# Kernel optimization log

Measured on AMD Instinct MI355X. Metric: run time of the kernel, lower is better.

Reference implementation:

```python
import jax, jax.numpy as jnp
import numpy as np

B, V, E, H, L = 8, 200, 40000, 128, 3


def setup_inputs() -> dict:
    key = jax.random.key(0)
    ks = jax.random.split(key, 24)
    s = 1.0 / np.sqrt(H)
    inp = {
        "x": jax.random.normal(ks[0], (B, V, 2), jnp.float32),
        "e": jax.random.uniform(ks[1], (B, E), jnp.float32),
        "edge_index": jax.random.randint(ks[2], (B, 2, E), 0, V),
        # Embedder
        "node_W": jax.random.normal(ks[3], (2, H), jnp.float32) * 0.5,
        "node_b": jnp.zeros((H,), jnp.float32),
        "edge_W": jax.random.normal(ks[4], (1, H), jnp.float32) * 0.5,
        "edge_b": jnp.zeros((H,), jnp.float32),
        # GCN layers (stacked over L)
        "U_W": jax.random.normal(ks[5], (L, H, H), jnp.float32) * s,
        "U_b": jnp.zeros((L, H), jnp.float32),
        "V_W": jax.random.normal(ks[6], (L, H, H), jnp.float32) * s,
        "V_b": jnp.zeros((L, H), jnp.float32),
        "A_W": jax.random.normal(ks[7], (L, H, H), jnp.float32) * s,
        "A_b": jnp.zeros((L, H), jnp.float32),
        "B_W": jax.random.normal(ks[8], (L, H, H), jnp.float32) * s,
        "B_b": jnp.zeros((L, H), jnp.float32),
        "C_W": jax.random.normal(ks[9], (L, H, H), jnp.float32) * s,
        "C_b": jnp.zeros((L, H), jnp.float32),
        # Out MLP: hidden -> hidden -> 2
        "out_W1": jax.random.normal(ks[10], (H, H), jnp.float32) * s,
        "out_b1": jnp.zeros((H,), jnp.float32),
        "out_W2": jax.random.normal(ks[11], (H, 2), jnp.float32) * s,
        "out_b2": jnp.zeros((2,), jnp.float32),
    }
    return inp


def reference(x, e, edge_index, node_W, node_b, edge_W, edge_b,
              U_W, U_b, V_W, V_b, A_W, A_b, B_W, B_b, C_W, C_b,
              out_W1, out_b1, out_W2, out_b2):
    n_nodes = x.shape[1]
    n_layers = U_W.shape[0]

    def per_graph(xi, ei, idx):
        # Embedder: coords (V,2)->(V,H), distances (E,)->(E,H)
        xh = xi @ node_W + node_b
        eh = ei[:, None] @ edge_W + edge_b
        src, dst = idx[0], idx[1]
        for l in range(n_layers):
            gate = jax.nn.sigmoid(eh)                       # (E,H) edge gates
            vx = xh @ V_W[l] + V_b[l]                       # (V,H)
            agg = jax.ops.segment_sum(gate * vx[src], dst,
                                      num_segments=n_nodes)  # (V,H)
            x_new = xh + jax.nn.relu(xh @ U_W[l] + U_b[l] + agg)
            eh = eh + jax.nn.relu(eh @ A_W[l] + A_b[l]
                                  + (xh @ B_W[l] + B_b[l])[src]
                                  + (xh @ C_W[l] + C_b[l])[dst])
            xh = x_new
        h = jax.nn.relu(eh @ out_W1 + out_b1)
        return jax.nn.sigmoid(h @ out_W2 + out_b2)           # (E,2)

    # batch loop in the original torch code -> vmap here
    return jax.vmap(per_graph)(x, e, edge_index)
```

## Files before the change

### kernel.cpp

```cpp
#include <hip/hip_runtime.h>
#include <hip/hip_bf16.h>

#define NB 8
#define NV 200
#define NE 40000
#define NH 128
#define NL 3
#define EBLK 157

typedef __attribute__((ext_vector_type(8))) __bf16 bf16x8;
typedef __attribute__((ext_vector_type(8))) short s16x8;
typedef __attribute__((ext_vector_type(4))) short s16x4;
typedef __attribute__((ext_vector_type(4))) float f32x4;

__device__ inline float sigmoidf_(float x){ return 1.0f/(1.0f + __expf(-x)); }

__device__ inline short f2b(float f){
  union{ float f; unsigned u; } v; v.f = f;
  unsigned u = v.u;
  u += 0x7fffu + ((u >> 16) & 1u);
  return (short)(u >> 16);
}
__device__ inline float b2f(short s){
  union{ unsigned u; float f; } v; v.u = ((unsigned)(unsigned short)s) << 16;
  return v.f;
}
__device__ inline void splitb(float x, short &hi, short &lo){
  hi = f2b(x);
  lo = f2b(x - b2f(hi));
}

__global__ __launch_bounds__(256) void k_embed_nodes(
    const float* __restrict__ x, const float* __restrict__ nW,
    const float* __restrict__ nb, float* __restrict__ xh)
{
  int i = blockIdx.x*256 + threadIdx.x;
  if (i >= NB*NV*NH) return;
  int h  = i & (NH-1);
  int bv = i >> 7;
  xh[i] = x[bv*2+0]*nW[h] + x[bv*2+1]*nW[NH+h] + nb[h];
}

__global__ __launch_bounds__(256) void k_trans_w(
    const float* __restrict__ AW, const float* __restrict__ oW1,
    short* __restrict__ Wt)
{
  int m = blockIdx.x;
  const float* src = (m < 3) ? (AW + m*NH*NH) : oW1;
  short* dhi = Wt + (size_t)m*NH*NH;
  short* dlo = Wt + (size_t)(4+m)*NH*NH;
  for (int i = threadIdx.x; i < NH*NH; i += 256){
    int n = i >> 7, k = i & 127;
    short hi, lo;
    splitb(src[k*NH + n], hi, lo);
    dhi[i] = hi; dlo[i] = lo;
  }
}

__global__ __launch_bounds__(256) void k_zero(int* __restrict__ p, int n){
  int i = blockIdx.x*256 + threadIdx.x;
  if (i < n) p[i] = 0;
}

__global__ __launch_bounds__(256) void k_count(const int* __restrict__ ei, int* __restrict__ counts){
  int i = blockIdx.x*256 + threadIdx.x;
  if (i >= NB*NE) return;
  int b = i / NE, e = i % NE;
  int dv = ei[b*2*NE + NE + e];
  atomicAdd(&counts[b*NV + dv], 1);
}

__global__ void k_scan(const int* __restrict__ counts, int* __restrict__ offs, int* __restrict__ cursor){
  int b = blockIdx.x;
  if (threadIdx.x == 0){
    int run = 0;
    for (int v=0; v<NV; v++){
      offs[b*(NV+1)+v] = run;
      cursor[b*NV+v]   = run;
      run += counts[b*NV+v];
    }
    offs[b*(NV+1)+NV] = run;
  }
}

__global__ __launch_bounds__(256) void k_scatter(const int* __restrict__ ei, int* __restrict__ cursor, int* __restrict__ csr){
  int i = blockIdx.x*256 + threadIdx.x;
  if (i >= NB*NE) return;
  int b = i / NE, e = i % NE;
  int dv = ei[b*2*NE + NE + e];
  int pos = atomicAdd(&cursor[b*NV + dv], 1);
  csr[(size_t)b*NE + pos] = e;
}

__global__ __launch_bounds__(256) void k_node_mm(
    float* __restrict__ xh, const float* __restrict__ agg,
    const float* __restrict__ VWl, const float* __restrict__ Vbl,
    const float* __restrict__ BWl, const float* __restrict__ Bbl,
    const float* __restrict__ CWl, const float* __restrict__ Cbl,
    const float* __restrict__ UWl, const float* __restrict__ Ubl,
    float* __restrict__ vx, float* __restrict__ bx,
    float* __restrict__ cx, float* __restrict__ ux,
    int do_update)
{
  __shared__ float sx[NH];
  int b = blockIdx.x / NV, v = blockIdx.x % NV;
  size_t row = (size_t)b*NV + v;
  float* xr = xh + row*NH;
  int ht = threadIdx.x;
  if (ht < NH){
    float xv = xr[ht];
    if (do_update){
      float u = ux[row*NH + ht];
      #pragma unroll
      for (int p=0;p<4;p++) u += agg[(size_t)p*NB*NV*NH + row*NH + ht];
      xv += u > 0.f ? u : 0.f;
      xr[ht] = xv;
    }
    sx[ht] = xv;
  }
  __syncthreads();
  #pragma unroll
  for (int pass=0; pass<2; pass++){
    int t = threadIdx.x + pass*256;
    int mat = t >> 7, h = t & 127;
    const float* W = (mat==0) ? VWl : (mat==1) ? BWl : (mat==2) ? CWl : UWl;
    const float* bs = (mat==0) ? Vbl : (mat==1) ? Bbl : (mat==2) ? Cbl : Ubl;
    float* op = (mat==0) ? vx : (mat==1) ? bx : (mat==2) ? cx : ux;
    float acc = bs[h];
    #pragma unroll 8
    for (int k=0;k<NH;k++) acc += sx[k]*W[k*NH + h];
    op[row*NH + h] = acc;
  }
}

__global__ __launch_bounds__(128) void k_agg(
    const float* __restrict__ eh, const float* __restrict__ evec,
    const float* __restrict__ eWe, const float* __restrict__ ebe,
    const float* __restrict__ vx, const int* __restrict__ ei,
    const int* __restrict__ csr, const int* __restrict__ offs,
    float* __restrict__ agg, int is_l0)
{
  int part = blockIdx.x & 3;
  int bv   = blockIdx.x >> 2;
  int b = bv / NV, v = bv % NV;
  int h = threadIdx.x;
  const int* srcp  = ei + b*2*NE;
  const int* csrg  = csr + (size_t)b*NE;
  const float* ehg = eh + (size_t)b*NE*NH;
  const float* evg = evec + (size_t)b*NE;
  const float* vxg = vx + (size_t)b*NV*NH;
  float wh = eWe[h], bh = ebe[h];
  int beg = offs[b*(NV+1)+v], end = offs[b*(NV+1)+v+1];
  int len = end - beg;
  int i    = beg + ((len*part) >> 2);
  int stop = beg + ((len*(part+1)) >> 2);
  float acc = 0.f;
  for (; i+8 <= stop; i += 8){
    int   eb[8], sb[8];
    float a[8], w[8];
    #pragma unroll
    for (int j=0;j<8;j++) eb[j] = csrg[i+j];
    #pragma unroll
    for (int j=0;j<8;j++) sb[j] = srcp[eb[j]];
    if (is_l0){
      #pragma unroll
      for (int j=0;j<8;j++) a[j] = evg[eb[j]]*wh + bh;
    } else {
      #pragma unroll
      for (int j=0;j<8;j++) a[j] = ehg[(size_t)eb[j]*NH + h];
    }
    #pragma unroll
    for (int j=0;j<8;j++) w[j] = vxg[sb[j]*NH + h];
    #pragma unroll
    for (int j=0;j<8;j++) acc += sigmoidf_(a[j]) * w[j];
  }
  for (; i < stop; i++){
    int e0 = csrg[i]; int s0 = srcp[e0];
    float a = is_l0 ? (evg[e0]*wh + bh) : ehg[(size_t)e0*NH+h];
    acc += sigmoidf_(a) * vxg[s0*NH+h];
  }
  agg[((size_t)part*NB*NV + (size_t)b*NV + v)*NH + h] = acc;
}

__global__ __launch_bounds__(512) void k_edge_update(
    float* __restrict__ eh, const short* __restrict__ Wt,
    const float* __restrict__ Ab, const float* __restrict__ bx,
    const float* __restrict__ cx, const int* __restrict__ ei,
    const float* __restrict__ evec, const float* __restrict__ eWe,
    const float* __restrict__ ebe, int is_l0)
{
  __shared__ short sW[2*NH*NH];
  const short* Whi = Wt;
  const short* Wlo = Wt + 4*NH*NH;
  {
    #pragma unroll
    for (int i=0;i<8;i++){
      int sidx = (threadIdx.x + i*512)*8;
      int p = sidx >> 14, r = sidx & 16383;
      int hh = r >> 7, kw = r & 127;
      const short* src = p ? Wlo : Whi;
      s16x8 vv = *(const s16x8*)(src + r);
      *(s16x8*)(sW + p*16384 + hh*128 + (kw ^ ((hh&7)<<3))) = vv;
    }
  }
  __syncthreads();

  int blk  = blockIdx.x % EBLK;
  int b    = blockIdx.x / EBLK;
  int wave = threadIdx.x >> 6;
  int lane = threadIdx.x & 63;
  int l15 = lane & 15, lg = lane >> 4;
  int eA = blk*256 + wave*32 + l15;
  int eB = eA + 16;
  int eAc = eA < NE ? eA : NE-1;
  int eBc = eB < NE ? eB : NE-1;
  float* ehg = eh + (size_t)b*NE*NH;
  const int* srcp = ei + b*2*NE;
  int svA = srcp[eAc], dvA = srcp[NE+eAc];
  int svB = srcp[eBc], dvB = srcp[NE+eBc];

  float evA = 0.f, evB = 0.f;
  f32x4 rA[8], rB[8];
  if (is_l0){
    evA = evec[(size_t)b*NE + eAc];
    evB = evec[(size_t)b*NE + eBc];
    #pragma unroll
    for (int kk=0;kk<4;kk++){
      f32x4 w0 = *(const f32x4*)(eWe + kk*32 + lg*8);
      f32x4 w1 = *(const f32x4*)(eWe + kk*32 + lg*8 + 4);
      f32x4 q0 = *(const f32x4*)(ebe + kk*32 + lg*8);
      f32x4 q1 = *(const f32x4*)(ebe + kk*32 + lg*8 + 4);
      #pragma unroll
      for (int j=0;j<4;j++){
        rA[2*kk][j]   = evA*w0[j] + q0[j];
        rA[2*kk+1][j] = evA*w1[j] + q1[j];
        rB[2*kk][j]   = evB*w0[j] + q0[j];
        rB[2*kk+1][j] = evB*w1[j] + q1[j];
      }
    }
  } else {
    const float* pA = ehg + (size_t)eAc*NH + lg*8;
    const float* pB = ehg + (size_t)eBc*NH + lg*8;
    #pragma unroll
    for (int kk=0;kk<4;kk++){
      rA[2*kk]   = *(const f32x4*)(pA + kk*32);
      rA[2*kk+1] = *(const f32x4*)(pA + kk*32 + 4);
    }
    #pragma unroll
    for (int kk=0;kk<4;kk++){
      rB[2*kk]   = *(const f32x4*)(pB + kk*32);
      rB[2*kk+1] = *(const f32x4*)(pB + kk*32 + 4);
    }
  }

  bf16x8 ahA[4], alA[4], ahB[4], alB[4];
  #pragma unroll
  for (int kk=0;kk<4;kk++){
    union{ short s[8]; bf16x8 v; } uh, ul;
    #pragma unroll
    for (int j=0;j<4;j++){
      splitb(rA[2*kk][j],   uh.s[j],   ul.s[j]);
      splitb(rA[2*kk+1][j], uh.s[4+j], ul.s[4+j]);
    }
    ahA[kk] = uh.v; alA[kk] = ul.v;
  }
  #pragma unroll
  for (int kk=0;kk<4;kk++){
    union{ short s[8]; bf16x8 v; } uh, ul;
    #pragma unroll
    for (int j=0;j<4;j++){
      splitb(rB[2*kk][j],   uh.s[j],   ul.s[j]);
      splitb(rB[2*kk+1][j], uh.s[4+j], ul.s[4+j]);
    }
    ahB[kk] = uh.v; alB[kk] = ul.v;
  }

  f32x4 accA[8], accB[8];
  #pragma unroll
  for (int n=0;n<8;n++){ accA[n] = (f32x4){0.f,0.f,0.f,0.f}; accB[n] = (f32x4){0.f,0.f,0.f,0.f}; }

  #pragma unroll
  for (int kk=0;kk<4;kk++){
    #pragma unroll
    for (int n=0;n<8;n++){
      int row = n*16 + l15;
      int cofs = (kk*32 + lg*8) ^ ((l15&7)<<3);
      union{ s16x8 s; bf16x8 v; } wh, wl;
      wh.s = *(const s16x8*)(sW + row*128 + cofs);
      wl.s = *(const s16x8*)(sW + 16384 + row*128 + cofs);
      accA[n] = __builtin_amdgcn_mfma_f32_16x16x32_bf16(wh.v, ahA[kk], accA[n], 0, 0, 0);
      accA[n] = __builtin_amdgcn_mfma_f32_16x16x32_bf16(wh.v, alA[kk], accA[n], 0, 0, 0);
      accA[n] = __builtin_amdgcn_mfma_f32_16x16x32_bf16(wl.v, ahA[kk], accA[n], 0, 0, 0);
      accB[n] = __builtin_amdgcn_mfma_f32_16x16x32_bf16(wh.v, ahB[kk], accB[n], 0, 0, 0);
      accB[n] = __builtin_amdgcn_mfma_f32_16x16x32_bf16(wh.v, alB[kk], accB[n], 0, 0, 0);
      accB[n] = __builtin_amdgcn_mfma_f32_16x16x32_bf16(wl.v, ahB[kk], accB[n], 0, 0, 0);
    }
  }

  const float* bxA = bx + ((size_t)b*NV + svA)*NH;
  const float* cxA = cx + ((size_t)b*NV + dvA)*NH;
  const float* bxB = bx + ((size_t)b*NV + svB)*NH;
  const float* cxB = cx + ((size_t)b*NV + dvB)*NH;
  float* ehA = ehg + (size_t)eAc*NH;
  float* ehB = ehg + (size_t)eBc*NH;
  #pragma unroll
  for (int n=0;n<8;n++){
    int h0 = n*16 + lg*4;
    f32x4 ab4 = *(const f32x4*)(Ab + h0);
    f32x4 bA = *(const f32x4*)(bxA + h0);
    f32x4 cA = *(const f32x4*)(cxA + h0);
    f32x4 bB = *(const f32x4*)(bxB + h0);
    f32x4 cB = *(const f32x4*)(cxB + h0);
    f32x4 oA, oB;
    if (is_l0){
      f32x4 w4 = *(const f32x4*)(eWe + h0);
      f32x4 q4 = *(const f32x4*)(ebe + h0);
      #pragma unroll
      for (int j=0;j<4;j++){ oA[j] = evA*w4[j] + q4[j]; oB[j] = evB*w4[j] + q4[j]; }
    } else {
      oA = *(const f32x4*)(ehA + h0);
      oB = *(const f32x4*)(ehB + h0);
    }
    f32x4 nA, nB;
    #pragma unroll
    for (int j=0;j<4;j++){
      float vA = accA[n][j] + ab4[j] + bA[j] + cA[j];
      vA = vA > 0.f ? vA : 0.f;
      nA[j] = oA[j] + vA;
      float vB = accB[n][j] + ab4[j] + bB[j] + cB[j];
      vB = vB > 0.f ? vB : 0.f;
      nB[j] = oB[j] + vB;
    }
    if (eA < NE) *(f32x4*)(ehA + h0) = nA;
    if (eB < NE) *(f32x4*)(ehB + h0) = nB;
  }
}

__global__ __launch_bounds__(512) void k_edge_out(
    const float* __restrict__ eh, const short* __restrict__ Wt,
    const float* __restrict__ Ab, const float* __restrict__ bx,
    const float* __restrict__ cx, const int* __restrict__ ei,
    const float* __restrict__ b1, const float* __restrict__ W2,
    const float* __restrict__ b2, float* __restrict__ out)
{
  __shared__ short sW[2*NH*NH];
  const short* Whi = Wt + 2*NH*NH;
  const short* Wlo = Wt + 6*NH*NH;
  {
    #pragma unroll
    for (int i=0;i<8;i++){
      int sidx = (threadIdx.x + i*512)*8;
      int p = sidx >> 14, r = sidx & 16383;
      int hh = r >> 7, kw = r & 127;
      const short* src = p ? Wlo : Whi;
      s16x8 vv = *(const s16x8*)(src + r);
      *(s16x8*)(sW + p*16384 + hh*128 + (kw ^ ((hh&7)<<3))) = vv;
    }
  }
  __syncthreads();

  int blk  = blockIdx.x % EBLK;
  int b    = blockIdx.x / EBLK;
  int wave = threadIdx.x >> 6;
  int lane = threadIdx.x & 63;
  int l15 = lane & 15, lg = lane >> 4;
  int eA = blk*256 + wave*32 + l15;
  int eB = eA + 16;
  int eAc = eA < NE ? eA : NE-1;
  int eBc = eB < NE ? eB : NE-1;
  const float* ehg = eh + (size_t)b*NE*NH;
  const int* srcp = ei + b*2*NE;
  int svA = srcp[eAc], dvA = srcp[NE+eAc];
  int svB = srcp[eBc], dvB = srcp[NE+eBc];

  const float* pA = ehg + (size_t)eAc*NH + lg*8;
  const float* pB = ehg + (size_t)eBc*NH + lg*8;
  f32x4 rA[8], rB[8];
  #pragma unroll
  for (int kk=0;kk<4;kk++){
    rA[2*kk]   = *(const f32x4*)(pA + kk*32);
    rA[2*kk+1] = *(const f32x4*)(pA + kk*32 + 4);
  }
  #pragma unroll
  for (int kk=0;kk<4;kk++){
    rB[2*kk]   = *(const f32x4*)(pB + kk*32);
    rB[2*kk+1] = *(const f32x4*)(pB + kk*32 + 4);
  }

  bf16x8 ahA[4], alA[4], ahB[4], alB[4];
  #pragma unroll
  for (int kk=0;kk<4;kk++){
    union{ short s[8]; bf16x8 v; } uh, ul;
    #pragma unroll
    for (int j=0;j<4;j++){
      splitb(rA[2*kk][j],   uh.s[j],   ul.s[j]);
      splitb(rA[2*kk+1][j], uh.s[4+j], ul.s[4+j]);
    }
    ahA[kk] = uh.v; alA[kk] = ul.v;
  }
  #pragma unroll
  for (int kk=0;kk<4;kk++){
    union{ short s[8]; bf16x8 v; } uh, ul;
    #pragma unroll
    for (int j=0;j<4;j++){
      splitb(rB[2*kk][j],   uh.s[j],   ul.s[j]);
      splitb(rB[2*kk+1][j], uh.s[4+j], ul.s[4+j]);
    }
    ahB[kk] = uh.v; alB[kk] = ul.v;
  }

  f32x4 accA[8], accB[8];
  #pragma unroll
  for (int n=0;n<8;n++){ accA[n] = (f32x4){0.f,0.f,0.f,0.f}; accB[n] = (f32x4){0.f,0.f,0.f,0.f}; }
  #pragma unroll
  for (int kk=0;kk<4;kk++){
    #pragma unroll
    for (int n=0;n<8;n++){
      int row = n*16 + l15;
      int cofs = (kk*32 + lg*8) ^ ((l15&7)<<3);
      union{ s16x8 s; bf16x8 v; } wh, wl;
      wh.s = *(const s16x8*)(sW + row*128 + cofs);
      wl.s = *(const s16x8*)(sW + 16384 + row*128 + cofs);
      accA[n] = __builtin_amdgcn_mfma_f32_16x16x32_bf16(wh.v, ahA[kk], accA[n], 0, 0, 0);
      accA[n] = __builtin_amdgcn_mfma_f32_16x16x32_bf16(wh.v, alA[kk], accA[n], 0, 0, 0);
      accA[n] = __builtin_amdgcn_mfma_f32_16x16x32_bf16(wl.v, ahA[kk], accA[n], 0, 0, 0);
      accB[n] = __builtin_amdgcn_mfma_f32_16x16x32_bf16(wh.v, ahB[kk], accB[n], 0, 0, 0);
      accB[n] = __builtin_amdgcn_mfma_f32_16x16x32_bf16(wh.v, alB[kk], accB[n], 0, 0, 0);
      accB[n] = __builtin_amdgcn_mfma_f32_16x16x32_bf16(wl.v, ahB[kk], accB[n], 0, 0, 0);
    }
  }

  f32x4 nAr[8], nBr[8];
  const float* bxA = bx + ((size_t)b*NV + svA)*NH;
  const float* cxA = cx + ((size_t)b*NV + dvA)*NH;
  const float* bxB = bx + ((size_t)b*NV + svB)*NH;
  const float* cxB = cx + ((size_t)b*NV + dvB)*NH;
  const float* ehA = ehg + (size_t)eAc*NH;
  const float* ehB = ehg + (size_t)eBc*NH;
  #pragma unroll
  for (int n=0;n<8;n++){
    int h0 = n*16 + lg*4;
    f32x4 ab4 = *(const f32x4*)(Ab + h0);
    f32x4 bA = *(const f32x4*)(bxA + h0);
    f32x4 cA = *(const f32x4*)(cxA + h0);
    f32x4 oA = *(const f32x4*)(ehA + h0);
    f32x4 bB = *(const f32x4*)(bxB + h0);
    f32x4 cB = *(const f32x4*)(cxB + h0);
    f32x4 oB = *(const f32x4*)(ehB + h0);
    #pragma unroll
    for (int j=0;j<4;j++){
      float vA = accA[n][j] + ab4[j] + bA[j] + cA[j];
      vA = vA > 0.f ? vA : 0.f;
      nAr[n][j] = oA[j] + vA;
      float vB = accB[n][j] + ab4[j] + bB[j] + cB[j];
      vB = vB > 0.f ? vB : 0.f;
      nBr[n][j] = oB[j] + vB;
    }
  }

  __syncthreads();
  {
    const short* W1hi = Wt + 3*NH*NH;
    const short* W1lo = Wt + 7*NH*NH;
    #pragma unroll
    for (int i=0;i<16;i++){
      int qd = threadIdx.x + i*512;
      int p = qd >> 12, rr = qd & 4095;
      int row = rr >> 5;
      int c0 = (rr & 31) << 2;
      int kk = c0 >> 5, lgs = (c0 >> 3) & 3, jhi = (c0 & 7) >> 2;
      int base = 32*kk + 16*jhi + 4*lgs;
      const short* src = p ? W1lo : W1hi;
      s16x4 v = *(const s16x4*)(src + row*128 + base);
      *(s16x4*)(sW + p*16384 + row*128 + (c0 ^ ((row&7)<<3))) = v;
    }
  }
  __syncthreads();

  bf16x8 qhA[4], qlA[4], qhB[4], qlB[4];
  #pragma unroll
  for (int kk=0;kk<4;kk++){
    union{ short s[8]; bf16x8 v; } uhA, ulA, uhB, ulB;
    #pragma unroll
    for (int j=0;j<8;j++){
      splitb(nAr[2*kk + (j>>2)][j&3], uhA.s[j], ulA.s[j]);
      splitb(nBr[2*kk + (j>>2)][j&3], uhB.s[j], ulB.s[j]);
    }
    qhA[kk] = uhA.v; qlA[kk] = ulA.v;
    qhB[kk] = uhB.v; qlB[kk] = ulB.v;
  }

  f32x4 acc2A[8], acc2B[8];
  #pragma unroll
  for (int n=0;n<8;n++){ acc2A[n] = (f32x4){0.f,0.f,0.f,0.f}; acc2B[n] = (f32x4){0.f,0.f,0.f,0.f}; }
  #pragma unroll
  for (int kk=0;kk<4;kk++){
    #pragma unroll
    for (int n=0;n<8;n++){
      int row = n*16 + l15;
      int cofs = (kk*32 + lg*8) ^ ((l15&7)<<3);
      union{ s16x8 s; bf16x8 v; } wh, wl;
      wh.s = *(const s16x8*)(sW + row*128 + cofs);
      wl.s = *(const s16x8*)(sW + 16384 + row*128 + cofs);
      acc2A[n] = __builtin_amdgcn_mfma_f32_16x16x32_bf16(wh.v, qhA[kk], acc2A[n], 0, 0, 0);
      acc2A[n] = __builtin_amdgcn_mfma_f32_16x16x32_bf16(wh.v, qlA[kk], acc2A[n], 0, 0, 0);
      acc2A[n] = __builtin_amdgcn_mfma_f32_16x16x32_bf16(wl.v, qhA[kk], acc2A[n], 0, 0, 0);
      acc2B[n] = __builtin_amdgcn_mfma_f32_16x16x32_bf16(wh.v, qhB[kk], acc2B[n], 0, 0, 0);
      acc2B[n] = __builtin_amdgcn_mfma_f32_16x16x32_bf16(wh.v, qlB[kk], acc2B[n], 0, 0, 0);
      acc2B[n] = __builtin_amdgcn_mfma_f32_16x16x32_bf16(wl.v, qhB[kk], acc2B[n], 0, 0, 0);
    }
  }

  float p0A = 0.f, p1A = 0.f, p0B = 0.f, p1B = 0.f;
  #pragma unroll
  for (int n=0;n<8;n++){
    int h0 = n*16 + lg*4;
    f32x4 b14 = *(const f32x4*)(b1 + h0);
    f32x4 wA  = *(const f32x4*)(W2 + h0*2);
    f32x4 wB  = *(const f32x4*)(W2 + h0*2 + 4);
    #pragma unroll
    for (int j=0;j<4;j++){
      float w20 = (j<2) ? wA[2*j]   : wB[2*(j-2)];
      float w21 = (j<2) ? wA[2*j+1] : wB[2*(j-2)+1];
      float hA = acc2A[n][j] + b14[j]; hA = hA > 0.f ? hA : 0.f;
      float hB = acc2B[n][j] + b14[j]; hB = hB > 0.f ? hB : 0.f;
      p0A += hA*w20; p1A += hA*w21;
      p0B += hB*w20; p1B += hB*w21;
    }
  }
  p0A += __shfl_xor(p0A, 16, 64); p0A += __shfl_xor(p0A, 32, 64);
  p1A += __shfl_xor(p1A, 16, 64); p1A += __shfl_xor(p1A, 32, 64);
  p0B += __shfl_xor(p0B, 16, 64); p0B += __shfl_xor(p0B, 32, 64);
  p1B += __shfl_xor(p1B, 16, 64); p1B += __shfl_xor(p1B, 32, 64);
  if (lg == 0){
    float bb0 = b2[0], bb1 = b2[1];
    if (eA < NE){
      float2 r; r.x = sigmoidf_(p0A + bb0); r.y = sigmoidf_(p1A + bb1);
      *(float2*)(out + ((size_t)b*NE + eA)*2) = r;
    }
    if (eB < NE){
      float2 r; r.x = sigmoidf_(p0B + bb0); r.y = sigmoidf_(p1B + bb1);
      *(float2*)(out + ((size_t)b*NE + eB)*2) = r;
    }
  }
}

extern "C" void kernel_launch(void* const* d_in, const int* in_sizes, int n_in,
                              void* d_out, int out_size, void* d_ws, size_t ws_size,
                              hipStream_t stream)
{
  const float* x   = (const float*)d_in[0];
  const float* e   = (const float*)d_in[1];
  const int*   ei  = (const int*)d_in[2];
  const float* nW  = (const float*)d_in[3];
  const float* nb  = (const float*)d_in[4];
  const float* eW  = (const float*)d_in[5];
  const float* eb  = (const float*)d_in[6];
  const float* UW  = (const float*)d_in[7];
  const float* Ub  = (const float*)d_in[8];
  const float* VW  = (const float*)d_in[9];
  const float* Vb  = (const float*)d_in[10];
  const float* AW  = (const float*)d_in[11];
  const float* Ab  = (const float*)d_in[12];
  const float* BW  = (const float*)d_in[13];
  const float* Bb  = (const float*)d_in[14];
  const float* CW  = (const float*)d_in[15];
  const float* Cb  = (const float*)d_in[16];
  const float* oW1 = (const float*)d_in[17];
  const float* ob1 = (const float*)d_in[18];
  const float* oW2 = (const float*)d_in[19];
  const float* ob2 = (const float*)d_in[20];
  float* out = (float*)d_out;

  char* ws = (char*)d_ws;
  size_t off = 0;
  auto alloc = [&](size_t bytes)->char*{
    char* p = ws + off;
    off += (bytes + 255) & ~(size_t)255;
    return p;
  };
  float* eh     = (float*)alloc((size_t)NB*NE*NH*4);
  float* xh     = (float*)alloc((size_t)NB*NV*NH*4);
  float* vx     = (float*)alloc((size_t)NB*NV*NH*4);
  float* bx     = (float*)alloc((size_t)NB*NV*NH*4);
  float* cx     = (float*)alloc((size_t)NB*NV*NH*4);
  float* ux     = (float*)alloc((size_t)NB*NV*NH*4);
  float* agg    = (float*)alloc((size_t)4*NB*NV*NH*4);
  short* Wt     = (short*)alloc((size_t)8*NH*NH*2);
  int* counts   = (int*)alloc((size_t)NB*NV*4);
  int* cursor   = (int*)alloc((size_t)NB*NV*4);
  int* offs     = (int*)alloc((size_t)NB*(NV+1)*4);
  int* csr      = (int*)alloc((size_t)NB*NE*4);
  (void)ws_size; (void)in_sizes; (void)n_in; (void)out_size;

  k_embed_nodes<<<(NB*NV*NH+255)/256, 256, 0, stream>>>(x, nW, nb, xh);
  k_trans_w<<<4, 256, 0, stream>>>(AW, oW1, Wt);
  k_zero<<<(NB*NV+255)/256, 256, 0, stream>>>(counts, NB*NV);
  k_count<<<(NB*NE+255)/256, 256, 0, stream>>>(ei, counts);
  k_scan<<<NB, 64, 0, stream>>>(counts, offs, cursor);
  k_scatter<<<(NB*NE+255)/256, 256, 0, stream>>>(ei, cursor, csr);

  for (int l=0; l<NL; l++){
    k_node_mm<<<NB*NV, 256, 0, stream>>>(xh, agg,
        VW + l*NH*NH, Vb + l*NH, BW + l*NH*NH, Bb + l*NH,
        CW + l*NH*NH, Cb + l*NH, UW + l*NH*NH, Ub + l*NH,
        vx, bx, cx, ux, l > 0 ? 1 : 0);
    if (l < NL-1)
      k_agg<<<NB*NV*4, 128, 0, stream>>>(eh, e, eW, eb, vx, ei, csr, offs, agg, l==0 ? 1 : 0);
    if (l < NL-1)
      k_edge_update<<<NB*EBLK, 512, 0, stream>>>(eh, Wt + l*NH*NH, Ab + l*NH, bx, cx, ei,
                                                 e, eW, eb, l==0 ? 1 : 0);
    else
      k_edge_out<<<NB*EBLK, 512, 0, stream>>>(eh, Wt, Ab + l*NH, bx, cx, ei,
                                              ob1, oW2, ob2, out);
  }
}
```

Baseline: 554.7 us.

## Halve edge-block size, keep only hi weights in LDS, read lo weights from global

```diff
diff --git a/kernel.cpp b/kernel.cpp
--- a/kernel.cpp
+++ b/kernel.cpp
@@ -6,11 +6,10 @@
 #define NE 40000
 #define NH 128
 #define NL 3
-#define EBLK 157
+#define EBLK 313
 
 typedef __attribute__((ext_vector_type(8))) __bf16 bf16x8;
 typedef __attribute__((ext_vector_type(8))) short s16x8;
-typedef __attribute__((ext_vector_type(4))) short s16x4;
 typedef __attribute__((ext_vector_type(4))) float f32x4;
 
 __device__ inline float sigmoidf_(float x){ return 1.0f/(1.0f + __expf(-x)); }
@@ -50,7 +49,14 @@
   short* dhi = Wt + (size_t)m*NH*NH;
   short* dlo = Wt + (size_t)(4+m)*NH*NH;
   for (int i = threadIdx.x; i < NH*NH; i += 256){
-    int n = i >> 7, k = i & 127;
+    int n = i >> 7, c = i & 127;
+    int k;
+    if (m < 3){
+      k = c;
+    } else {
+      int kk = c >> 5, lg = (c >> 3) & 3, jh = (c >> 2) & 1, jl = c & 3;
+      k = 32*kk + 16*jh + 4*lg + jl;
+    }
     short hi, lo;
     splitb(src[k*NH + n], hi, lo);
     dhi[i] = hi; dlo[i] = lo;
@@ -182,25 +188,23 @@
   agg[((size_t)part*NB*NV + (size_t)b*NV + v)*NH + h] = acc;
 }
 
-__global__ __launch_bounds__(512) void k_edge_update(
+__global__ __launch_bounds__(256) void k_edge_update(
     float* __restrict__ eh, const short* __restrict__ Wt,
     const float* __restrict__ Ab, const float* __restrict__ bx,
     const float* __restrict__ cx, const int* __restrict__ ei,
     const float* __restrict__ evec, const float* __restrict__ eWe,
     const float* __restrict__ ebe, int is_l0)
 {
-  __shared__ short sW[2*NH*NH];
+  __shared__ short sW[NH*NH];
   const short* Whi = Wt;
   const short* Wlo = Wt + 4*NH*NH;
   {
     #pragma unroll
     for (int i=0;i<8;i++){
-      int sidx = (threadIdx.x + i*512)*8;
-      int p = sidx >> 14, r = sidx & 16383;
-      int hh = r >> 7, kw = r & 127;
-      const short* src = p ? Wlo : Whi;
-      s16x8 vv = *(const s16x8*)(src + r);
-      *(s16x8*)(sW + p*16384 + hh*128 + (kw ^ ((hh&7)<<3))) = vv;
+      int sidx = (threadIdx.x + i*256)*8;
+      int hh = sidx >> 7, kw = sidx & 127;
+      s16x8 vv = *(const s16x8*)(Whi + sidx);
+      *(s16x8*)(sW + hh*128 + (kw ^ ((hh&7)<<3))) = vv;
     }
   }
   __syncthreads();
@@ -210,7 +214,7 @@
   int wave = threadIdx.x >> 6;
   int lane = threadIdx.x & 63;
   int l15 = lane & 15, lg = lane >> 4;
-  int eA = blk*256 + wave*32 + l15;
+  int eA = blk*128 + wave*32 + l15;
   int eB = eA + 16;
   int eAc = eA < NE ? eA : NE-1;
   int eBc = eB < NE ? eB : NE-1;
@@ -287,7 +291,7 @@
       int cofs = (kk*32 + lg*8) ^ ((l15&7)<<3);
       union{ s16x8 s; bf16x8 v; } wh, wl;
       wh.s = *(const s16x8*)(sW + row*128 + cofs);
-      wl.s = *(const s16x8*)(sW + 16384 + row*128 + cofs);
+      wl.s = *(const s16x8*)(Wlo + row*NH + kk*32 + lg*8);
       accA[n] = __builtin_amdgcn_mfma_f32_16x16x32_bf16(wh.v, ahA[kk], accA[n], 0, 0, 0);
       accA[n] = __builtin_amdgcn_mfma_f32_16x16x32_bf16(wh.v, alA[kk], accA[n], 0, 0, 0);
       accA[n] = __builtin_amdgcn_mfma_f32_16x16x32_bf16(wl.v, ahA[kk], accA[n], 0, 0, 0);
@@ -336,25 +340,25 @@
   }
 }
 
-__global__ __launch_bounds__(512) void k_edge_out(
+__global__ __launch_bounds__(256) void k_edge_out(
     const float* __restrict__ eh, const short* __restrict__ Wt,
     const float* __restrict__ Ab, const float* __restrict__ bx,
     const float* __restrict__ cx, const int* __restrict__ ei,
     const float* __restrict__ b1, const float* __restrict__ W2,
     const float* __restrict__ b2, float* __restrict__ out)
 {
-  __shared__ short sW[2*NH*NH];
-  const short* Whi = Wt + 2*NH*NH;
-  const short* Wlo = Wt + 6*NH*NH;
+  __shared__ short sW[NH*NH];
+  const short* Whi  = Wt + 2*NH*NH;
+  const short* Wlo  = Wt + 6*NH*NH;
+  const short* W1hi = Wt + 3*NH*NH;
+  const short* W1lo = Wt + 7*NH*NH;
   {
     #pragma unroll
     for (int i=0;i<8;i++){
-      int sidx = (threadIdx.x + i*512)*8;
-      int p = sidx >> 14, r = sidx & 16383;
-      int hh = r >> 7, kw = r & 127;
-      const short* src = p ? Wlo : Whi;
-      s16x8 vv = *(const s16x8*)(src + r);
-      *(s16x8*)(sW + p*16384 + hh*128 + (kw ^ ((hh&7)<<3))) = vv;
+      int sidx = (threadIdx.x + i*256)*8;
+      int hh = sidx >> 7, kw = sidx & 127;
+      s16x8 vv = *(const s16x8*)(Whi + sidx);
+      *(s16x8*)(sW + hh*128 + (kw ^ ((hh&7)<<3))) = vv;
     }
   }
   __syncthreads();
@@ -364,7 +368,7 @@
   int wave = threadIdx.x >> 6;
   int lane = threadIdx.x & 63;
   int l15 = lane & 15, lg = lane >> 4;
-  int eA = blk*256 + wave*32 + l15;
+  int eA = blk*128 + wave*32 + l15;
   int eB = eA + 16;
   int eAc = eA < NE ? eA : NE-1;
   int eBc = eB < NE ? eB : NE-1;
@@ -420,7 +424,7 @@
       int cofs = (kk*32 + lg*8) ^ ((l15&7)<<3);
       union{ s16x8 s; bf16x8 v; } wh, wl;
       wh.s = *(const s16x8*)(sW + row*128 + cofs);
-      wl.s = *(const s16x8*)(sW + 16384 + row*128 + cofs);
+      wl.s = *(const s16x8*)(Wlo + row*NH + kk*32 + lg*8);
       accA[n] = __builtin_amdgcn_mfma_f32_16x16x32_bf16(wh.v, ahA[kk], accA[n], 0, 0, 0);
       accA[n] = __builtin_amdgcn_mfma_f32_16x16x32_bf16(wh.v, alA[kk], accA[n], 0, 0, 0);
       accA[n] = __builtin_amdgcn_mfma_f32_16x16x32_bf16(wl.v, ahA[kk], accA[n], 0, 0, 0);
@@ -460,19 +464,12 @@
 
   __syncthreads();
   {
-    const short* W1hi = Wt + 3*NH*NH;
-    const short* W1lo = Wt + 7*NH*NH;
-    #pragma unroll
-    for (int i=0;i<16;i++){
-      int qd = threadIdx.x + i*512;
-      int p = qd >> 12, rr = qd & 4095;
-      int row = rr >> 5;
-      int c0 = (rr & 31) << 2;
-      int kk = c0 >> 5, lgs = (c0 >> 3) & 3, jhi = (c0 & 7) >> 2;
-      int base = 32*kk + 16*jhi + 4*lgs;
-      const short* src = p ? W1lo : W1hi;
-      s16x4 v = *(const s16x4*)(src + row*128 + base);
-      *(s16x4*)(sW + p*16384 + row*128 + (c0 ^ ((row&7)<<3))) = v;
+    #pragma unroll
+    for (int i=0;i<8;i++){
+      int sidx = (threadIdx.x + i*256)*8;
+      int hh = sidx >> 7, kw = sidx & 127;
+      s16x8 vv = *(const s16x8*)(W1hi + sidx);
+      *(s16x8*)(sW + hh*128 + (kw ^ ((hh&7)<<3))) = vv;
     }
   }
   __syncthreads();
@@ -501,7 +498,7 @@
       int cofs = (kk*32 + lg*8) ^ ((l15&7)<<3);
       union{ s16x8 s; bf16x8 v; } wh, wl;
       wh.s = *(const s16x8*)(sW + row*128 + cofs);
-      wl.s = *(const s16x8*)(sW + 16384 + row*128 + cofs);
+      wl.s = *(const s16x8*)(W1lo + row*NH + kk*32 + lg*8);
       acc2A[n] = __builtin_amdgcn_mfma_f32_16x16x32_bf16(wh.v, qhA[kk], acc2A[n], 0, 0, 0);
       acc2A[n] = __builtin_amdgcn_mfma_f32_16x16x32_bf16(wh.v, qlA[kk], acc2A[n], 0, 0, 0);
       acc2A[n] = __builtin_amdgcn_mfma_f32_16x16x32_bf16(wl.v, qhA[kk], acc2A[n], 0, 0, 0);
@@ -608,10 +605,10 @@
     if (l < NL-1)
       k_agg<<<NB*NV*4, 128, 0, stream>>>(eh, e, eW, eb, vx, ei, csr, offs, agg, l==0 ? 1 : 0);
     if (l < NL-1)
-      k_edge_update<<<NB*EBLK, 512, 0, stream>>>(eh, Wt + l*NH*NH, Ab + l*NH, bx, cx, ei,
+      k_edge_update<<<NB*EBLK, 256, 0, stream>>>(eh, Wt + l*NH*NH, Ab + l*NH, bx, cx, ei,
                                                  e, eW, eb, l==0 ? 1 : 0);
     else
-      k_edge_out<<<NB*EBLK, 512, 0, stream>>>(eh, Wt, Ab + l*NH, bx, cx, ei,
+      k_edge_out<<<NB*EBLK, 256, 0, stream>>>(eh, Wt, Ab + l*NH, bx, cx, ei,
                                               ob1, oW2, ob2, out);
   }
 }
```

Result: slower. 653.5 us (+17.8%).

## Preload both edge-out weight matrices into LDS and fuse epilogue with bf16 split

Applied to the files above, without the earlier changes.

```diff
diff --git a/kernel.cpp b/kernel.cpp
--- a/kernel.cpp
+++ b/kernel.cpp
@@ -10,7 +10,6 @@
 
 typedef __attribute__((ext_vector_type(8))) __bf16 bf16x8;
 typedef __attribute__((ext_vector_type(8))) short s16x8;
-typedef __attribute__((ext_vector_type(4))) short s16x4;
 typedef __attribute__((ext_vector_type(4))) float f32x4;
 
 __device__ inline float sigmoidf_(float x){ return 1.0f/(1.0f + __expf(-x)); }
@@ -50,7 +49,14 @@
   short* dhi = Wt + (size_t)m*NH*NH;
   short* dlo = Wt + (size_t)(4+m)*NH*NH;
   for (int i = threadIdx.x; i < NH*NH; i += 256){
-    int n = i >> 7, k = i & 127;
+    int n = i >> 7, c = i & 127;
+    int k;
+    if (m < 3){
+      k = c;
+    } else {
+      int kk = c >> 5, lg = (c >> 3) & 3, jh = (c >> 2) & 1, jl = c & 3;
+      k = 32*kk + 16*jh + 4*lg + jl;
+    }
     short hi, lo;
     splitb(src[k*NH + n], hi, lo);
     dhi[i] = hi; dlo[i] = lo;
@@ -343,16 +349,19 @@
     const float* __restrict__ b1, const float* __restrict__ W2,
     const float* __restrict__ b2, float* __restrict__ out)
 {
-  __shared__ short sW[2*NH*NH];
-  const short* Whi = Wt + 2*NH*NH;
-  const short* Wlo = Wt + 6*NH*NH;
+  __shared__ short sW[4*NH*NH];
   {
-    #pragma unroll
-    for (int i=0;i<8;i++){
+    const short* A2hi = Wt + 2*NH*NH;
+    const short* A2lo = Wt + 6*NH*NH;
+    const short* W1hi = Wt + 3*NH*NH;
+    const short* W1lo = Wt + 7*NH*NH;
+    #pragma unroll
+    for (int i=0;i<16;i++){
       int sidx = (threadIdx.x + i*512)*8;
-      int p = sidx >> 14, r = sidx & 16383;
+      int p = i >> 2;
+      int r = sidx & 16383;
       int hh = r >> 7, kw = r & 127;
-      const short* src = p ? Wlo : Whi;
+      const short* src = (p==0)? A2hi : (p==1)? A2lo : (p==2)? W1hi : W1lo;
       s16x8 vv = *(const s16x8*)(src + r);
       *(s16x8*)(sW + p*16384 + hh*128 + (kw ^ ((hh&7)<<3))) = vv;
     }
@@ -430,61 +439,38 @@
     }
   }
 
-  f32x4 nAr[8], nBr[8];
   const float* bxA = bx + ((size_t)b*NV + svA)*NH;
   const float* cxA = cx + ((size_t)b*NV + dvA)*NH;
   const float* bxB = bx + ((size_t)b*NV + svB)*NH;
   const float* cxB = cx + ((size_t)b*NV + dvB)*NH;
   const float* ehA = ehg + (size_t)eAc*NH;
   const float* ehB = ehg + (size_t)eBc*NH;
-  #pragma unroll
-  for (int n=0;n<8;n++){
-    int h0 = n*16 + lg*4;
-    f32x4 ab4 = *(const f32x4*)(Ab + h0);
-    f32x4 bA = *(const f32x4*)(bxA + h0);
-    f32x4 cA = *(const f32x4*)(cxA + h0);
-    f32x4 oA = *(const f32x4*)(ehA + h0);
-    f32x4 bB = *(const f32x4*)(bxB + h0);
-    f32x4 cB = *(const f32x4*)(cxB + h0);
-    f32x4 oB = *(const f32x4*)(ehB + h0);
-    #pragma unroll
-    for (int j=0;j<4;j++){
-      float vA = accA[n][j] + ab4[j] + bA[j] + cA[j];
-      vA = vA > 0.f ? vA : 0.f;
-      nAr[n][j] = oA[j] + vA;
-      float vB = accB[n][j] + ab4[j] + bB[j] + cB[j];
-      vB = vB > 0.f ? vB : 0.f;
-      nBr[n][j] = oB[j] + vB;
-    }
-  }
-
-  __syncthreads();
-  {
-    const short* W1hi = Wt + 3*NH*NH;
-    const short* W1lo = Wt + 7*NH*NH;
-    #pragma unroll
-    for (int i=0;i<16;i++){
-      int qd = threadIdx.x + i*512;
-      int p = qd >> 12, rr = qd & 4095;
-      int row = rr >> 5;
-      int c0 = (rr & 31) << 2;
-      int kk = c0 >> 5, lgs = (c0 >> 3) & 3, jhi = (c0 & 7) >> 2;
-      int base = 32*kk + 16*jhi + 4*lgs;
-      const short* src = p ? W1lo : W1hi;
-      s16x4 v = *(const s16x4*)(src + row*128 + base);
-      *(s16x4*)(sW + p*16384 + row*128 + (c0 ^ ((row&7)<<3))) = v;
-    }
-  }
-  __syncthreads();
-
   bf16x8 qhA[4], qlA[4], qhB[4], qlB[4];
   #pragma unroll
   for (int kk=0;kk<4;kk++){
     union{ short s[8]; bf16x8 v; } uhA, ulA, uhB, ulB;
     #pragma unroll
-    for (int j=0;j<8;j++){
-      splitb(nAr[2*kk + (j>>2)][j&3], uhA.s[j], ulA.s[j]);
-      splitb(nBr[2*kk + (j>>2)][j&3], uhB.s[j], ulB.s[j]);
+    for (int half=0; half<2; half++){
+      int n = 2*kk + half;
+      int h0 = n*16 + lg*4;
+      f32x4 ab4 = *(const f32x4*)(Ab + h0);
+      f32x4 bA4 = *(const f32x4*)(bxA + h0);
+      f32x4 cA4 = *(const f32x4*)(cxA + h0);
+      f32x4 oA4 = *(const f32x4*)(ehA + h0);
+      f32x4 bB4 = *(const f32x4*)(bxB + h0);
+      f32x4 cB4 = *(const f32x4*)(cxB + h0);
+      f32x4 oB4 = *(const f32x4*)(ehB + h0);
+      #pragma unroll
+      for (int j=0;j<4;j++){
+        float vA = accA[n][j] + ab4[j] + bA4[j] + cA4[j];
+        vA = vA > 0.f ? vA : 0.f;
+        float e3A = oA4[j] + vA;
+        splitb(e3A, uhA.s[half*4+j], ulA.s[half*4+j]);
+        float vB = accB[n][j] + ab4[j] + bB4[j] + cB4[j];
+        vB = vB > 0.f ? vB : 0.f;
+        float e3B = oB4[j] + vB;
+        splitb(e3B, uhB.s[half*4+j], ulB.s[half*4+j]);
+      }
     }
     qhA[kk] = uhA.v; qlA[kk] = ulA.v;
     qhB[kk] = uhB.v; qlB[kk] = ulB.v;
@@ -500,8 +486,8 @@
       int row = n*16 + l15;
       int cofs = (kk*32 + lg*8) ^ ((l15&7)<<3);
       union{ s16x8 s; bf16x8 v; } wh, wl;
-      wh.s = *(const s16x8*)(sW + row*128 + cofs);
-      wl.s = *(const s16x8*)(sW + 16384 + row*128 + cofs);
+      wh.s = *(const s16x8*)(sW + 2*16384 + row*128 + cofs);
+      wl.s = *(const s16x8*)(sW + 3*16384 + row*128 + cofs);
       acc2A[n] = __builtin_amdgcn_mfma_f32_16x16x32_bf16(wh.v, qhA[kk], acc2A[n], 0, 0, 0);
       acc2A[n] = __builtin_amdgcn_mfma_f32_16x16x32_bf16(wh.v, qlA[kk], acc2A[n], 0, 0, 0);
       acc2A[n] = __builtin_amdgcn_mfma_f32_16x16x32_bf16(wl.v, qhA[kk], acc2A[n], 0, 0, 0);
```

Result: faster. 532.0 us (median of 2 runs) (-4.1%).
